# Kernel tuning notes

Hardware: AMD Instinct MI355X
Metric: run time of the kernel (lower is better)

## Reference

```python
import jax, jax.numpy as jnp
import numpy as np

B, S, D, H, E, K = 4, 2048, 512, 2048, 8, 2


def setup_inputs() -> dict:
    key = jax.random.key(0)
    k0, k1, k2, k3 = jax.random.split(key, 4)
    return {
        "x": jax.random.normal(k0, (B, S, D), jnp.float32),
        "router_w": jax.random.normal(k1, (E, D), jnp.float32) * 0.02,
        "router_b": jnp.zeros((E,), jnp.float32),
        "w1": jax.random.normal(k2, (E, D, H), jnp.float32) * 0.02,
        "b1": jnp.zeros((E, H), jnp.float32),
        "w2": jax.random.normal(k3, (E, H, D), jnp.float32) * 0.02,
        "b2": jnp.zeros((E, D), jnp.float32),
        "top_k": K,
    }


def reference(x, router_w, router_b, w1, b1, w2, b2, top_k):
    # x: [B, S, D]; eval mode (no router noise, no dropout)
    Bb, Ss, Dd = x.shape
    Ee = w1.shape[0]
    xf = x.reshape(-1, Dd)                                   # [T, D], T = B*S
    router_logits = xf @ router_w.T + router_b               # [T, E]
    top_v, top_i = jax.lax.top_k(router_logits, top_k)       # [T, K]
    rw = jax.nn.softmax(top_v, axis=-1)                      # [T, K]
    # combine[t, e] = sum_k rw[t, k] * (top_i[t, k] == e); zero for unrouted experts
    combine = jnp.sum(jax.nn.one_hot(top_i, Ee, dtype=xf.dtype) * rw[..., None], axis=1)  # [T, E]
    out = jnp.zeros_like(xf)
    for e in range(Ee):  # fixed small expert count; each iter is a dense GEMM pair
        h = jax.nn.gelu(xf @ w1[e] + b1[e], approximate=False)  # exact erf GELU like torch nn.GELU
        y = h @ w2[e] + b2[e]                                   # [T, D]
        out = out + combine[:, e:e + 1] * y
    return out.reshape(Bb, Ss, Dd), router_logits
```

## Files before the change

kernel.cpp:

```cpp
#include <hip/hip_runtime.h>
#include <hip/hip_bf16.h>

#define TTOK 8192
#define DDIM 512
#define HDIM 2048
#define NEXP 8
#define RBLK 256
#define RTOK (TTOK / RBLK)

typedef __bf16 bf16x8 __attribute__((ext_vector_type(8)));
typedef float f32x4 __attribute__((ext_vector_type(4)));
typedef unsigned short us8 __attribute__((ext_vector_type(8)));

__device__ __forceinline__ unsigned short f2bf(float f) {
  unsigned int u = __builtin_bit_cast(unsigned int, f);
  u += 0x7fffu + ((u >> 16) & 1u);
  return (unsigned short)(u >> 16);
}

__device__ __forceinline__ void gll16(const void* g, void* l) {
  __builtin_amdgcn_global_load_lds(
      (__attribute__((address_space(1))) void*)g,
      (__attribute__((address_space(3))) void*)l, 16, 0, 0);
}

__global__ __launch_bounds__(256) void k_router(
    const float* __restrict__ x, const float* __restrict__ rw,
    const float* __restrict__ rb, float* __restrict__ logits,
    unsigned short* __restrict__ xb,
    short* __restrict__ texp, unsigned short* __restrict__ tpos,
    float* __restrict__ tgate, int* __restrict__ blockcnt) {
  __shared__ int lcnt[NEXP];
  const int tid = threadIdx.x, wid = tid >> 6, lane = tid & 63;
  if (tid < NEXP) lcnt[tid] = 0;
  __syncthreads();
  float4 w0[NEXP], w1[NEXP];
  float rbv[NEXP];
#pragma unroll
  for (int e = 0; e < NEXP; ++e) {
    const float4* wp = (const float4*)(rw + e * DDIM);
    w0[e] = wp[lane * 2];
    w1[e] = wp[lane * 2 + 1];
    rbv[e] = rb[e];
  }
  const int tbase = blockIdx.x * RTOK;
  for (int it = 0; it < RTOK / 4; ++it) {
    const int t = tbase + it * 4 + wid;
    const float4* xr = (const float4*)(x + (size_t)t * DDIM);
    float4 v0 = xr[lane * 2], v1 = xr[lane * 2 + 1];
    us8 o;
    o[0] = f2bf(v0.x); o[1] = f2bf(v0.y); o[2] = f2bf(v0.z); o[3] = f2bf(v0.w);
    o[4] = f2bf(v1.x); o[5] = f2bf(v1.y); o[6] = f2bf(v1.z); o[7] = f2bf(v1.w);
    *(us8*)(xb + (size_t)t * DDIM + lane * 8) = o;
    float a[NEXP];
#pragma unroll
    for (int e = 0; e < NEXP; ++e)
      a[e] = v0.x * w0[e].x + v0.y * w0[e].y + v0.z * w0[e].z + v0.w * w0[e].w +
             v1.x * w1[e].x + v1.y * w1[e].y + v1.z * w1[e].z + v1.w * w1[e].w;
#pragma unroll
    for (int off = 32; off > 0; off >>= 1)
#pragma unroll
      for (int e = 0; e < NEXP; ++e) a[e] += __shfl_xor(a[e], off, 64);
    if (lane == 0) {
      float lg[NEXP];
#pragma unroll
      for (int e = 0; e < NEXP; ++e) lg[e] = a[e] + rbv[e];
      float4 s0, s1;
      s0.x = lg[0]; s0.y = lg[1]; s0.z = lg[2]; s0.w = lg[3];
      s1.x = lg[4]; s1.y = lg[5]; s1.z = lg[6]; s1.w = lg[7];
      ((float4*)(logits + t * NEXP))[0] = s0;
      ((float4*)(logits + t * NEXP))[1] = s1;
      int i0 = 0; float m0 = lg[0];
#pragma unroll
      for (int e = 1; e < NEXP; ++e) if (lg[e] > m0) { m0 = lg[e]; i0 = e; }
      int i1 = 0; float m1 = -3.4e38f;
#pragma unroll
      for (int e = 0; e < NEXP; ++e) if (e != i0 && lg[e] > m1) { m1 = lg[e]; i1 = e; }
      float e1 = expf(m1 - m0);
      float inv = 1.0f / (1.0f + e1);
      int p0 = atomicAdd(&lcnt[i0], 1);
      int p1 = atomicAdd(&lcnt[i1], 1);
      texp[t * 2] = (short)i0;     tpos[t * 2] = (unsigned short)p0;     tgate[t * 2] = inv;
      texp[t * 2 + 1] = (short)i1; tpos[t * 2 + 1] = (unsigned short)p1; tgate[t * 2 + 1] = e1 * inv;
    }
  }
  __syncthreads();
  if (tid < NEXP) blockcnt[blockIdx.x * NEXP + tid] = lcnt[tid];
}

__global__ void k_offsets(const int* __restrict__ blockcnt, int* __restrict__ blockbase,
                          int* __restrict__ counts, int* __restrict__ offsets) {
  const int e = threadIdx.x;
  if (e < NEXP) {
    int run = 0;
#pragma unroll 8
    for (int b = 0; b < RBLK; ++b) {
      blockbase[b * NEXP + e] = run;
      run += blockcnt[b * NEXP + e];
    }
    counts[e] = run;
  }
  __syncthreads();
  if (e == 0) {
    int s = 0;
    for (int q = 0; q < NEXP; ++q) { offsets[q] = s; s += counts[q]; }
  }
}

__global__ void k_scatter(const short* __restrict__ texp, const unsigned short* __restrict__ tpos,
                          const float* __restrict__ tgate, const int* __restrict__ blockbase,
                          int* __restrict__ toklist, float* __restrict__ gates) {
  const int t = blockIdx.x * 256 + threadIdx.x;
  const int b = t / RTOK;
#pragma unroll
  for (int k = 0; k < 2; ++k) {
    const int e = (int)texp[t * 2 + k];
    const int pos = blockbase[b * NEXP + e] + (int)tpos[t * 2 + k];
    toklist[e * TTOK + pos] = t;
    gates[e * TTOK + pos] = tgate[t * 2 + k];
  }
}

__global__ void k_transpose(const float* __restrict__ in, unsigned short* __restrict__ out,
                            int R, int C) {
  __shared__ float tile[32][33];
  const int e = blockIdx.z;
  const float* ine = in + (size_t)e * R * C;
  unsigned short* oute = out + (size_t)e * R * C;
  const int c0 = blockIdx.x * 32, r0 = blockIdx.y * 32;
  const int tx = threadIdx.x, ty = threadIdx.y;
#pragma unroll
  for (int i = 0; i < 32; i += 8)
    tile[ty + i][tx] = ine[(size_t)(r0 + ty + i) * C + (c0 + tx)];
  __syncthreads();
#pragma unroll
  for (int i = 0; i < 32; i += 8)
    oute[(size_t)(c0 + ty + i) * R + (r0 + tx)] = f2bf(tile[tx][ty + i]);
}

template <int PHASE>
__global__ __launch_bounds__(256, 2) void k_gemm(
    const unsigned short* __restrict__ A, const unsigned short* __restrict__ Bt,
    const float* __restrict__ bias, const int* __restrict__ counts,
    const int* __restrict__ offsets, const int* __restrict__ toklist,
    const float* __restrict__ gates, unsigned short* __restrict__ Hout,
    float* __restrict__ Out) {
  constexpr int K = (PHASE == 1) ? DDIM : HDIM;
  constexpr int NN = (PHASE == 1) ? HDIM : DDIM;
  constexpr int KB = K * 2;

  const int e = blockIdx.z;
  const int cnt = counts[e];
  const int m0 = blockIdx.y * 128;
  if (m0 >= cnt) return;
  const int n0 = blockIdx.x * 128;
  const int off = offsets[e];

  __shared__ alignas(16) unsigned char smem[32768];

  const int tid = threadIdx.x;
  const int wid = tid >> 6, lane = tid & 63;

  const char* asrc[4];
  const char* bsrc[4];
  unsigned adst[4], bdst[4];
#pragma unroll
  for (int i = 0; i < 4; ++i) {
    const int c = i * 4 + wid;
    const int r = c * 8 + (lane >> 3);
    const int cs = ((lane & 7) * 16) ^ ((r & 7) << 4);
    int mrow = m0 + r; if (mrow > cnt - 1) mrow = cnt - 1;
    if (PHASE == 1) {
      const int tok = toklist[(e << 13) + mrow];
      asrc[i] = (const char*)A + (size_t)tok * (DDIM * 2) + cs;
    } else {
      asrc[i] = (const char*)A + (size_t)(off + mrow) * KB + cs;
    }
    bsrc[i] = (const char*)Bt + (size_t)e * NN * KB + (size_t)(n0 + r) * KB + cs;
    adst[i] = c * 1024;
    bdst[i] = 16384 + c * 1024;
  }

  f32x4 acc[4][4] = {};

  const int wr = wid >> 1, wc = wid & 1;
  const int lr = lane & 15, lk = lane >> 4;

  for (int k0 = 0; k0 < K; k0 += 64) {
#pragma unroll
    for (int i = 0; i < 4; ++i) gll16(asrc[i] + k0 * 2, smem + adst[i]);
#pragma unroll
    for (int i = 0; i < 4; ++i) gll16(bsrc[i] + k0 * 2, smem + bdst[i]);
    __syncthreads();
#pragma unroll
    for (int kk = 0; kk < 2; ++kk) {
      bf16x8 af[4], bv[4];
#pragma unroll
      for (int mi = 0; mi < 4; ++mi) {
        const int r = wr * 64 + mi * 16 + lr;
        const int byteo = r * 128 + ((kk * 64 + lk * 16) ^ ((r & 7) << 4));
        af[mi] = *(const bf16x8*)(smem + byteo);
      }
#pragma unroll
      for (int ni = 0; ni < 4; ++ni) {
        const int r = wc * 64 + ni * 16 + lr;
        const int byteo = 16384 + r * 128 + ((kk * 64 + lk * 16) ^ ((r & 7) << 4));
        bv[ni] = *(const bf16x8*)(smem + byteo);
      }
#pragma unroll
      for (int mi = 0; mi < 4; ++mi)
#pragma unroll
        for (int ni = 0; ni < 4; ++ni)
          acc[mi][ni] = __builtin_amdgcn_mfma_f32_16x16x32_bf16(af[mi], bv[ni], acc[mi][ni], 0, 0, 0);
    }
    __syncthreads();
  }

  const int lq = lane >> 4;
  if (PHASE == 1) {
#pragma unroll
    for (int mi = 0; mi < 4; ++mi) {
#pragma unroll
      for (int ni = 0; ni < 4; ++ni) {
        const int n = n0 + wc * 64 + ni * 16 + lr;
        const float bv_ = bias[e * NN + n];
#pragma unroll
        for (int r2 = 0; r2 < 4; ++r2) {
          const int m = m0 + wr * 64 + mi * 16 + lq * 4 + r2;
          if (m < cnt) {
            const float xv = acc[mi][ni][r2] + bv_;
            const float g = 0.5f * xv * (1.0f + erff(xv * 0.70710678118f));
            Hout[(size_t)(off + m) * HDIM + n] = f2bf(g);
          }
        }
      }
    }
  } else {
#pragma unroll
    for (int mi = 0; mi < 4; ++mi) {
#pragma unroll
      for (int r2 = 0; r2 < 4; ++r2) {
        const int m = m0 + wr * 64 + mi * 16 + lq * 4 + r2;
        if (m < cnt) {
          const int tok = toklist[(e << 13) + m];
          const float g = gates[(e << 13) + m];
#pragma unroll
          for (int ni = 0; ni < 4; ++ni) {
            const int n = n0 + wc * 64 + ni * 16 + lr;
            const float y = acc[mi][ni][r2] + bias[e * NN + n];
            atomicAdd(Out + (size_t)tok * DDIM + n, g * y);
          }
        }
      }
    }
  }
}

extern "C" void kernel_launch(void* const* d_in, const int* in_sizes, int n_in,
                              void* d_out, int out_size, void* d_ws, size_t ws_size,
                              hipStream_t stream) {
  (void)in_sizes; (void)n_in; (void)out_size; (void)ws_size;
  const float* x  = (const float*)d_in[0];
  const float* rw = (const float*)d_in[1];
  const float* rb = (const float*)d_in[2];
  const float* w1 = (const float*)d_in[3];
  const float* b1 = (const float*)d_in[4];
  const float* w2 = (const float*)d_in[5];
  const float* b2 = (const float*)d_in[6];
  float* out = (float*)d_out;
  float* logits = out + (size_t)TTOK * DDIM;

  char* ws = (char*)d_ws;
  unsigned short* xb  = (unsigned short*)(ws + 0);
  unsigned short* w1t = (unsigned short*)(ws + 8388608);
  unsigned short* w2t = (unsigned short*)(ws + 25165824);
  unsigned short* h   = (unsigned short*)(ws + 41943040);
  int*   toklist = (int*)(ws + 109051904);
  float* gates   = (float*)(ws + 109314048);
  int*   counts  = (int*)(ws + 109576192);
  int*   offsets = (int*)(ws + 109576224);
  char* rsc = ws + 41943040;
  short*          texp      = (short*)(rsc + 0);
  unsigned short* tpos      = (unsigned short*)(rsc + 32768);
  float*          tgate     = (float*)(rsc + 65536);
  int*            blockcnt  = (int*)(rsc + 131072);
  int*            blockbase = (int*)(rsc + 139264);

  hipMemsetAsync(out, 0, (size_t)TTOK * DDIM * sizeof(float), stream);

  k_router<<<RBLK, 256, 0, stream>>>(x, rw, rb, logits, xb, texp, tpos, tgate, blockcnt);
  k_transpose<<<dim3(HDIM / 32, DDIM / 32, NEXP), dim3(32, 8), 0, stream>>>(w1, w1t, DDIM, HDIM);
  k_transpose<<<dim3(DDIM / 32, HDIM / 32, NEXP), dim3(32, 8), 0, stream>>>(w2, w2t, HDIM, DDIM);
  k_offsets<<<1, 64, 0, stream>>>(blockcnt, blockbase, counts, offsets);
  k_scatter<<<TTOK / 256, 256, 0, stream>>>(texp, tpos, tgate, blockbase, toklist, gates);

  k_gemm<1><<<dim3(HDIM / 128, TTOK / 128, NEXP), 256, 0, stream>>>(
      xb, w1t, b1, counts, offsets, toklist, gates, h, nullptr);
  k_gemm<2><<<dim3(DDIM / 128, TTOK / 128, NEXP), 256, 0, stream>>>(
      h, w2t, b2, counts, offsets, toklist, gates, nullptr, out);
}
```

Baseline: 320.9 us.

## Double-buffer LDS tiles in expert GEMM and interleave experts in 1D grid

The GEMM main loop now prefetches the next K-tile into a second 32KB LDS buffer while the MFMAs consume the current one, dropping one barrier per iteration. The goal is to overlap global-to-LDS loads with compute. The grid is flattened to 1D with the expert index in the low bits, so neighbouring blocks work on different experts and early-exit blocks spread more evenly across CUs. LDS use doubles to 64KB per block, which may limit how many blocks can be resident at once under launch_bounds(256,2).

```diff
diff --git a/kernel.cpp b/kernel.cpp
--- a/kernel.cpp
+++ b/kernel.cpp
@@ -148,15 +148,20 @@
   constexpr int K = (PHASE == 1) ? DDIM : HDIM;
   constexpr int NN = (PHASE == 1) ? HDIM : DDIM;
   constexpr int KB = K * 2;
-
-  const int e = blockIdx.z;
+  constexpr int NX = NN / 128;
+  constexpr int NXSH = (PHASE == 1) ? 4 : 2;
+  constexpr int NT = K / 64;
+
+  const int id = blockIdx.x;
+  const int e = id & 7;
+  const int p = id >> 3;
   const int cnt = counts[e];
-  const int m0 = blockIdx.y * 128;
+  const int m0 = (p >> NXSH) * 128;
   if (m0 >= cnt) return;
-  const int n0 = blockIdx.x * 128;
+  const int n0 = (p & (NX - 1)) * 128;
   const int off = offsets[e];
 
-  __shared__ alignas(16) unsigned char smem[32768];
+  __shared__ alignas(16) unsigned char smem[65536];
 
   const int tid = threadIdx.x;
   const int wid = tid >> 6, lane = tid & 63;
@@ -186,25 +191,35 @@
   const int wr = wid >> 1, wc = wid & 1;
   const int lr = lane & 15, lk = lane >> 4;
 
-  for (int k0 = 0; k0 < K; k0 += 64) {
-#pragma unroll
-    for (int i = 0; i < 4; ++i) gll16(asrc[i] + k0 * 2, smem + adst[i]);
-#pragma unroll
-    for (int i = 0; i < 4; ++i) gll16(bsrc[i] + k0 * 2, smem + bdst[i]);
-    __syncthreads();
+#pragma unroll
+  for (int i = 0; i < 4; ++i) gll16(asrc[i], smem + adst[i]);
+#pragma unroll
+  for (int i = 0; i < 4; ++i) gll16(bsrc[i], smem + bdst[i]);
+  __syncthreads();
+
+  for (int t = 0; t < NT; ++t) {
+    const unsigned cur = (unsigned)(t & 1) * 32768u;
+    if (t + 1 < NT) {
+      const unsigned nxt = cur ^ 32768u;
+      const int kb = (t + 1) * 128;
+#pragma unroll
+      for (int i = 0; i < 4; ++i) gll16(asrc[i] + kb, smem + nxt + adst[i]);
+#pragma unroll
+      for (int i = 0; i < 4; ++i) gll16(bsrc[i] + kb, smem + nxt + bdst[i]);
+    }
 #pragma unroll
     for (int kk = 0; kk < 2; ++kk) {
       bf16x8 af[4], bv[4];
 #pragma unroll
       for (int mi = 0; mi < 4; ++mi) {
         const int r = wr * 64 + mi * 16 + lr;
-        const int byteo = r * 128 + ((kk * 64 + lk * 16) ^ ((r & 7) << 4));
+        const unsigned byteo = cur + r * 128 + ((kk * 64 + lk * 16) ^ ((r & 7) << 4));
         af[mi] = *(const bf16x8*)(smem + byteo);
       }
 #pragma unroll
       for (int ni = 0; ni < 4; ++ni) {
         const int r = wc * 64 + ni * 16 + lr;
-        const int byteo = 16384 + r * 128 + ((kk * 64 + lk * 16) ^ ((r & 7) << 4));
+        const unsigned byteo = cur + 16384 + r * 128 + ((kk * 64 + lk * 16) ^ ((r & 7) << 4));
         bv[ni] = *(const bf16x8*)(smem + byteo);
       }
 #pragma unroll
@@ -213,7 +228,7 @@
         for (int ni = 0; ni < 4; ++ni)
           acc[mi][ni] = __builtin_amdgcn_mfma_f32_16x16x32_bf16(af[mi], bv[ni], acc[mi][ni], 0, 0, 0);
     }
-    __syncthreads();
+    if (t + 1 < NT) __syncthreads();
   }
 
   const int lq = lane >> 4;
@@ -294,8 +309,8 @@
   k_offsets<<<1, 64, 0, stream>>>(blockcnt, blockbase, counts, offsets);
   k_scatter<<<TTOK / 256, 256, 0, stream>>>(texp, tpos, tgate, blockbase, toklist, gates);
 
-  k_gemm<1><<<dim3(HDIM / 128, TTOK / 128, NEXP), 256, 0, stream>>>(
+  k_gemm<1><<<(HDIM / 128) * (TTOK / 128) * NEXP, 256, 0, stream>>>(
       xb, w1t, b1, counts, offsets, toklist, gates, h, nullptr);
-  k_gemm<2><<<dim3(DDIM / 128, TTOK / 128, NEXP), 256, 0, stream>>>(
+  k_gemm<2><<<(DDIM / 128) * (TTOK / 128) * NEXP, 256, 0, stream>>>(
       h, w2t, b2, counts, offsets, toklist, gates, nullptr, out);
 }
```

After: 349.7 us. +9.0%, slower.
